# Kernel tuning notes

Hardware: AMD Instinct MI355X
Metric: run time of the kernel (lower is better)

Reference implementation:

```python
import jax, jax.numpy as jnp
import numpy as np

N_NODES = 50000
N_EDGES = 800000
IN_FEATS = 256
OUT_FEATS = 64


def setup_inputs() -> dict:
    key = jax.random.key(0)
    k1, k2, k3, k4, k5, k6 = jax.random.split(key, 6)
    h = jax.random.normal(k1, (N_NODES, IN_FEATS), dtype=jnp.float32)
    norm = jax.random.uniform(k2, (N_NODES, 1), dtype=jnp.float32)
    weight = jax.random.normal(k3, (IN_FEATS, OUT_FEATS), dtype=jnp.float32) * (1.0 / np.sqrt(OUT_FEATS))
    bias = jax.random.normal(k4, (OUT_FEATS,), dtype=jnp.float32) * (1.0 / np.sqrt(OUT_FEATS))
    src = jax.random.randint(k5, (N_EDGES,), 0, N_NODES, dtype=jnp.int32)
    dst = jax.random.randint(k6, (N_EDGES,), 0, N_NODES, dtype=jnp.int32)
    return {"h": h, "norm": norm, "weight": weight, "bias": bias, "src": src, "dst": dst}


def reference(h, norm, weight, bias, src, dst):
    # h: [N, in_feats] -> linear transform
    hw = h @ weight                      # [N, out_feats]
    hw = hw * norm                       # pre-aggregation norm scale
    # update_all(copy_u, sum): out[v] = sum_{(u,v) in E} hw[u]
    msgs = hw[src]                       # [E, out_feats] gather
    agg = jax.ops.segment_sum(msgs, dst, num_segments=N_NODES)  # [N, out_feats]
    out = agg * norm                     # post-aggregation norm scale
    out = out + bias
    return jax.nn.relu(out)
```

## Files before the change

### kernel.cpp

```cpp
#include <hip/hip_runtime.h>

#define NN 50000
#define NE 800000
#define KF 256
#define MF 64

#define NBK 782
#define SB 60
#define EPB 14336
#define EPT 14
#define CAP 1536
#define GEMMB 196
#define OVF_CAP 4096

typedef __attribute__((ext_vector_type(8))) short short8;
typedef __attribute__((ext_vector_type(4))) float f32x4;

static __device__ __forceinline__ unsigned short f2bf(float x) {
  unsigned int u = __float_as_uint(x);
  u += 0x7FFF + ((u >> 16) & 1);
  return (unsigned short)(u >> 16);
}
static __device__ __forceinline__ float bf2f(unsigned short u) {
  return __uint_as_float(((unsigned int)u) << 16);
}

__global__ __launch_bounds__(1024) void scatter_gemm(
    const int* __restrict__ src, const int* __restrict__ dst,
    int* __restrict__ gCur, int* __restrict__ gOvf,
    unsigned int* __restrict__ ovf, int* __restrict__ eidx,
    const float* __restrict__ h, const float* __restrict__ W,
    const float* __restrict__ norm, unsigned short* __restrict__ hwb) {
  const int t = threadIdx.x;

  if (blockIdx.x >= SB) {
    __shared__ unsigned short wt[16384];
    if (blockIdx.x == SB && t < 64) hwb[(size_t)NN * MF + t] = 0;
    for (int f = t; f < 2048; f += 1024) {
      const int m = f & 15;
      const int quad = (f >> 4) & 3;
      const int nt = (f >> 6) & 3;
      const int k0i = f >> 8;
      const int n = nt * 16 + m;
      const int kb = k0i * 32 + quad * 8;
      short8 p;
#pragma unroll
      for (int j = 0; j < 8; ++j) p[j] = (short)f2bf(W[(kb + j) * MF + n]);
      *(short8*)(wt + (size_t)f * 8) = p;
    }

    const int sub = t >> 8;
    const int tt = t & 255;
    const int lane = tt & 63;
    const int wv = tt >> 6;
    const int m = lane & 15;
    const int quad = lane >> 4;
    const int row0 = (blockIdx.x - SB) * 256 + sub * 64;
    const int arow = row0 + wv * 16 + m;
    const int rowc = (arow < NN) ? arow : (NN - 1);
    const float4* ap = (const float4*)(h + (size_t)rowc * KF + quad * 8);

    float4 a[16];
#pragma unroll
    for (int k = 0; k < 8; ++k) {
      a[2 * k] = ap[k * 8];
      a[2 * k + 1] = ap[k * 8 + 1];
    }
    __builtin_amdgcn_sched_barrier(0);

    short8 af[8];
#pragma unroll
    for (int k = 0; k < 8; ++k) {
      const float4 a0 = a[2 * k];
      const float4 a1 = a[2 * k + 1];
      af[k][0] = (short)f2bf(a0.x); af[k][1] = (short)f2bf(a0.y);
      af[k][2] = (short)f2bf(a0.z); af[k][3] = (short)f2bf(a0.w);
      af[k][4] = (short)f2bf(a1.x); af[k][5] = (short)f2bf(a1.y);
      af[k][6] = (short)f2bf(a1.z); af[k][7] = (short)f2bf(a1.w);
    }
    __syncthreads();

    f32x4 acc[4];
#pragma unroll
    for (int i = 0; i < 4; ++i) acc[i] = (f32x4){0.f, 0.f, 0.f, 0.f};

    const short8* wp = (const short8*)wt;
#pragma unroll
    for (int k0i = 0; k0i < 8; ++k0i) {
      const short8* wk = wp + k0i * 256 + lane;
#pragma unroll
      for (int nt = 0; nt < 4; ++nt) {
        const short8 bf = wk[nt * 64];
        acc[nt] = __builtin_amdgcn_mfma_f32_16x16x32_bf16(af[k0i], bf, acc[nt], 0, 0, 0);
      }
    }

    const int gm0 = row0 + wv * 16 + quad * 4;
    float nrm[4];
#pragma unroll
    for (int r = 0; r < 4; ++r) nrm[r] = (gm0 + r < NN) ? norm[gm0 + r] : 0.f;
#pragma unroll
    for (int nt = 0; nt < 4; ++nt) {
#pragma unroll
      for (int r = 0; r < 4; ++r) {
        const int gm = gm0 + r;
        if (gm < NN) hwb[(size_t)gm * MF + nt * 16 + m] = f2bf(acc[nt][r] * nrm[r]);
      }
    }
    return;
  }

  __shared__ int hh[NBK];
  __shared__ int bb[NBK];
  const int base = (int)blockIdx.x * EPB;
  unsigned int ev[EPT];
#pragma unroll
  for (int i = 0; i < EPT; ++i) {
    const int e = base + i * 1024 + t;
    ev[i] = (e < NE) ? (((unsigned)src[e] << 16) | (unsigned)dst[e])
                     : 0xFFFFFFFFu;
  }
  for (int i = t; i < NBK; i += 1024) hh[i] = 0;
  __syncthreads();
#pragma unroll
  for (int i = 0; i < EPT; ++i)
    if (ev[i] != 0xFFFFFFFFu) atomicAdd(&hh[(ev[i] & 0xFFFFu) >> 6], 1);
  __syncthreads();
  for (int i = t; i < NBK; i += 1024) {
    const int c = hh[i];
    bb[i] = c ? atomicAdd(&gCur[i], c) : 0;
  }
  __syncthreads();
#pragma unroll
  for (int i = 0; i < EPT; ++i) {
    const unsigned v = ev[i];
    if (v != 0xFFFFFFFFu) {
      const int d = (int)(v & 0xFFFFu);
      const int bk = d >> 6;
      const int p = atomicAdd(&bb[bk], 1);
      if (p < CAP) {
        eidx[(size_t)bk * CAP + p] = (int)((v >> 16) << 6) | (d & 63);
      } else {
        const int o = atomicAdd(gOvf, 1);
        if (o < OVF_CAP) ovf[o] = v;
      }
    }
  }
}

__global__ __launch_bounds__(1024) void sort_gather(
    const int* __restrict__ gCur, const int* __restrict__ gOvf,
    const unsigned int* __restrict__ ovf, const int* __restrict__ eidx,
    const unsigned short* __restrict__ hwb, const float* __restrict__ norm,
    const float* __restrict__ bias, float* __restrict__ out) {
  __shared__ int hcnt[64];
  __shared__ int sBeg[64];
  __shared__ int sCur[64];
  __shared__ int pEnd[64];
  __shared__ int sE[2048];
  const int t = threadIdx.x;
  const int g = blockIdx.x;
  int cnt = gCur[g];
  cnt = (cnt < CAP) ? cnt : CAP;
  cnt = __builtin_amdgcn_readfirstlane(cnt);
  const int* ep = eidx + (size_t)g * CAP;
  if (t < 64) hcnt[t] = 0;
  __syncthreads();
  int v0 = -1, v1 = -1;
  if (t < cnt) {
    v0 = ep[t];
    atomicAdd(&hcnt[v0 & 63], 1);
  }
  if (t + 1024 < cnt) {
    v1 = ep[t + 1024];
    atomicAdd(&hcnt[v1 & 63], 1);
  }
  __syncthreads();
  if (t < 64) {
    const int v = hcnt[t];
    const int pc = (v + 7) & ~7;
    int incl = pc;
#pragma unroll
    for (int off = 1; off < 64; off <<= 1) {
      const int uu = __shfl_up(incl, off, 64);
      if (t >= off) incl += uu;
    }
    const int beg = incl - pc;
    sBeg[t] = beg;
    sCur[t] = beg;
    hcnt[t] = beg + v;
    pEnd[t] = beg + pc;
  }
  __syncthreads();
  if (v0 >= 0) sE[atomicAdd(&sCur[v0 & 63], 1)] = v0 >> 6;
  if (v1 >= 0) sE[atomicAdd(&sCur[v1 & 63], 1)] = v1 >> 6;
  if (t < 64) {
    for (int j = hcnt[t]; j < pEnd[t]; ++j) sE[j] = NN;
  }
  __syncthreads();

  const int lane = t & 63;
  const int wv = t >> 6;
  const float bi = bias[lane];
  const int novf = __builtin_amdgcn_readfirstlane(*gOvf);
#pragma unroll
  for (int nl = wv; nl < 64; nl += 16) {
    const int vtx = (g << 6) + nl;
    if (vtx >= NN) continue;
    const float nv = norm[vtx];
    const int s0i = __builtin_amdgcn_readfirstlane(sBeg[nl]);
    const int e0i = __builtin_amdgcn_readfirstlane(pEnd[nl]);
    float acc = 0.f;
    int i = s0i;
    for (; i + 16 <= e0i; i += 16) {
      int ss[16];
#pragma unroll
      for (int j = 0; j < 16; ++j) ss[j] = sE[i + j];
      unsigned short xs[16];
#pragma unroll
      for (int j = 0; j < 16; ++j) xs[j] = hwb[(size_t)ss[j] * MF + lane];
      __builtin_amdgcn_sched_barrier(0);
      float p0 = 0.f, p1 = 0.f, p2 = 0.f, p3 = 0.f;
#pragma unroll
      for (int j = 0; j < 16; j += 4) {
        p0 += bf2f(xs[j]);
        p1 += bf2f(xs[j + 1]);
        p2 += bf2f(xs[j + 2]);
        p3 += bf2f(xs[j + 3]);
      }
      acc += (p0 + p1) + (p2 + p3);
    }
    if (i < e0i) {
      const int s0 = sE[i], s1 = sE[i + 1], s2 = sE[i + 2], s3 = sE[i + 3];
      const int s4 = sE[i + 4], s5 = sE[i + 5], s6 = sE[i + 6], s7 = sE[i + 7];
      const unsigned short x0 = hwb[(size_t)s0 * MF + lane];
      const unsigned short x1 = hwb[(size_t)s1 * MF + lane];
      const unsigned short x2 = hwb[(size_t)s2 * MF + lane];
      const unsigned short x3 = hwb[(size_t)s3 * MF + lane];
      const unsigned short x4 = hwb[(size_t)s4 * MF + lane];
      const unsigned short x5 = hwb[(size_t)s5 * MF + lane];
      const unsigned short x6 = hwb[(size_t)s6 * MF + lane];
      const unsigned short x7 = hwb[(size_t)s7 * MF + lane];
      acc += bf2f(x0); acc += bf2f(x1); acc += bf2f(x2); acc += bf2f(x3);
      acc += bf2f(x4); acc += bf2f(x5); acc += bf2f(x6); acc += bf2f(x7);
    }
    if (novf > 0) {
      const int nn = (novf < OVF_CAP) ? novf : OVF_CAP;
      for (int ii = 0; ii < nn; ++ii) {
        const unsigned v = ovf[ii];
        if ((int)(v & 0xFFFFu) == vtx)
          acc += bf2f(hwb[(size_t)(v >> 16) * MF + lane]);
      }
    }
    const float o = acc * nv + bi;
    out[(size_t)vtx * MF + lane] = fmaxf(o, 0.f);
  }
}

extern "C" void kernel_launch(void* const* d_in, const int* in_sizes, int n_in,
                              void* d_out, int out_size, void* d_ws, size_t ws_size,
                              hipStream_t stream) {
  const float* h = (const float*)d_in[0];
  const float* norm = (const float*)d_in[1];
  const float* W = (const float*)d_in[2];
  const float* bias = (const float*)d_in[3];
  const int* src = (const int*)d_in[4];
  const int* dst = (const int*)d_in[5];
  float* out = (float*)d_out;

  unsigned short* hwb = (unsigned short*)d_ws;
  int* gCur = (int*)(hwb + (size_t)(NN + 1) * MF);
  int* gOvf = gCur + NBK;
  unsigned int* ovf = (unsigned int*)(gOvf + 1);
  int* eidx = (int*)(ovf + OVF_CAP);
  const size_t need = (size_t)(NN + 1) * MF * 2 +
                      ((size_t)NBK + 1 + OVF_CAP + (size_t)NBK * CAP) * 4;
  if (ws_size < need) return;

  hipMemsetAsync(gCur, 0, (NBK + 1) * sizeof(int), stream);
  scatter_gemm<<<SB + GEMMB, 1024, 0, stream>>>(src, dst, gCur, gOvf, ovf,
                                                eidx, h, W, norm, hwb);
  sort_gather<<<NBK, 1024, 0, stream>>>(gCur, gOvf, ovf, eidx, hwb, norm, bias,
                                        out);
}
```

Before: 130.5 us.

## Merge scatter and GEMM roles into every block across 256 blocks

Previously 60 blocks did edge bucketing and 196 separate blocks did the bf16 MFMA GEMM. Now all 256 blocks bucket a 3125-edge slice each, and the first 196 then also run the GEMM tile, with shared memory unioned between the two phases. This spreads the serial-heavy scatter work (fewer edges per block, fewer global atomics per block) over more CUs to shorten the critical path. The cost is that GEMM blocks must finish scattering before starting their matmul, which serialises the two phases within each block.

```diff
diff --git a/kernel.cpp b/kernel.cpp
--- a/kernel.cpp
+++ b/kernel.cpp
@@ -6,9 +6,8 @@
 #define MF 64
 
 #define NBK 782
-#define SB 60
-#define EPB 14336
-#define EPT 14
+#define NB 256
+#define EPBK 3125
 #define CAP 1536
 #define GEMMB 196
 #define OVF_CAP 4096
@@ -24,6 +23,14 @@
 static __device__ __forceinline__ float bf2f(unsigned short u) {
   return __uint_as_float(((unsigned int)u) << 16);
 }
+
+union SMem1 {
+  unsigned short wt[16384];
+  struct {
+    int hh[NBK];
+    int bb[NBK];
+  } sc;
+};
 
 __global__ __launch_bounds__(1024) void scatter_gemm(
     const int* __restrict__ src, const int* __restrict__ dst,
@@ -31,119 +38,117 @@
     unsigned int* __restrict__ ovf, int* __restrict__ eidx,
     const float* __restrict__ h, const float* __restrict__ W,
     const float* __restrict__ norm, unsigned short* __restrict__ hwb) {
+  __shared__ SMem1 u;
   const int t = threadIdx.x;
 
-  if (blockIdx.x >= SB) {
-    __shared__ unsigned short wt[16384];
-    if (blockIdx.x == SB && t < 64) hwb[(size_t)NN * MF + t] = 0;
-    for (int f = t; f < 2048; f += 1024) {
-      const int m = f & 15;
-      const int quad = (f >> 4) & 3;
-      const int nt = (f >> 6) & 3;
-      const int k0i = f >> 8;
-      const int n = nt * 16 + m;
-      const int kb = k0i * 32 + quad * 8;
-      short8 p;
-#pragma unroll
-      for (int j = 0; j < 8; ++j) p[j] = (short)f2bf(W[(kb + j) * MF + n]);
-      *(short8*)(wt + (size_t)f * 8) = p;
-    }
-
-    const int sub = t >> 8;
-    const int tt = t & 255;
-    const int lane = tt & 63;
-    const int wv = tt >> 6;
-    const int m = lane & 15;
-    const int quad = lane >> 4;
-    const int row0 = (blockIdx.x - SB) * 256 + sub * 64;
-    const int arow = row0 + wv * 16 + m;
-    const int rowc = (arow < NN) ? arow : (NN - 1);
-    const float4* ap = (const float4*)(h + (size_t)rowc * KF + quad * 8);
-
-    float4 a[16];
-#pragma unroll
-    for (int k = 0; k < 8; ++k) {
-      a[2 * k] = ap[k * 8];
-      a[2 * k + 1] = ap[k * 8 + 1];
-    }
-    __builtin_amdgcn_sched_barrier(0);
-
-    short8 af[8];
-#pragma unroll
-    for (int k = 0; k < 8; ++k) {
-      const float4 a0 = a[2 * k];
-      const float4 a1 = a[2 * k + 1];
-      af[k][0] = (short)f2bf(a0.x); af[k][1] = (short)f2bf(a0.y);
-      af[k][2] = (short)f2bf(a0.z); af[k][3] = (short)f2bf(a0.w);
-      af[k][4] = (short)f2bf(a1.x); af[k][5] = (short)f2bf(a1.y);
-      af[k][6] = (short)f2bf(a1.z); af[k][7] = (short)f2bf(a1.w);
-    }
-    __syncthreads();
-
-    f32x4 acc[4];
-#pragma unroll
-    for (int i = 0; i < 4; ++i) acc[i] = (f32x4){0.f, 0.f, 0.f, 0.f};
-
-    const short8* wp = (const short8*)wt;
-#pragma unroll
-    for (int k0i = 0; k0i < 8; ++k0i) {
-      const short8* wk = wp + k0i * 256 + lane;
-#pragma unroll
-      for (int nt = 0; nt < 4; ++nt) {
-        const short8 bf = wk[nt * 64];
-        acc[nt] = __builtin_amdgcn_mfma_f32_16x16x32_bf16(af[k0i], bf, acc[nt], 0, 0, 0);
-      }
-    }
-
-    const int gm0 = row0 + wv * 16 + quad * 4;
-    float nrm[4];
-#pragma unroll
-    for (int r = 0; r < 4; ++r) nrm[r] = (gm0 + r < NN) ? norm[gm0 + r] : 0.f;
-#pragma unroll
-    for (int nt = 0; nt < 4; ++nt) {
-#pragma unroll
-      for (int r = 0; r < 4; ++r) {
-        const int gm = gm0 + r;
-        if (gm < NN) hwb[(size_t)gm * MF + nt * 16 + m] = f2bf(acc[nt][r] * nrm[r]);
-      }
-    }
-    return;
-  }
-
-  __shared__ int hh[NBK];
-  __shared__ int bb[NBK];
-  const int base = (int)blockIdx.x * EPB;
-  unsigned int ev[EPT];
-#pragma unroll
-  for (int i = 0; i < EPT; ++i) {
-    const int e = base + i * 1024 + t;
-    ev[i] = (e < NE) ? (((unsigned)src[e] << 16) | (unsigned)dst[e])
-                     : 0xFFFFFFFFu;
-  }
-  for (int i = t; i < NBK; i += 1024) hh[i] = 0;
-  __syncthreads();
-#pragma unroll
-  for (int i = 0; i < EPT; ++i)
-    if (ev[i] != 0xFFFFFFFFu) atomicAdd(&hh[(ev[i] & 0xFFFFu) >> 6], 1);
+  if (blockIdx.x == 0 && t < 64) hwb[(size_t)NN * MF + t] = 0;
+  const int base = (int)blockIdx.x * EPBK;
+  unsigned int ev[4];
+#pragma unroll
+  for (int i = 0; i < 4; ++i) {
+    const int idx = i * 1024 + t;
+    ev[i] = (idx < EPBK)
+                ? (((unsigned)src[base + idx] << 16) | (unsigned)dst[base + idx])
+                : 0xFFFFFFFFu;
+  }
+  for (int i = t; i < NBK; i += 1024) u.sc.hh[i] = 0;
+  __syncthreads();
+#pragma unroll
+  for (int i = 0; i < 4; ++i)
+    if (ev[i] != 0xFFFFFFFFu) atomicAdd(&u.sc.hh[(ev[i] & 0xFFFFu) >> 6], 1);
   __syncthreads();
   for (int i = t; i < NBK; i += 1024) {
-    const int c = hh[i];
-    bb[i] = c ? atomicAdd(&gCur[i], c) : 0;
-  }
-  __syncthreads();
-#pragma unroll
-  for (int i = 0; i < EPT; ++i) {
+    const int c = u.sc.hh[i];
+    u.sc.bb[i] = c ? atomicAdd(&gCur[i], c) : 0;
+  }
+  __syncthreads();
+#pragma unroll
+  for (int i = 0; i < 4; ++i) {
     const unsigned v = ev[i];
     if (v != 0xFFFFFFFFu) {
       const int d = (int)(v & 0xFFFFu);
       const int bk = d >> 6;
-      const int p = atomicAdd(&bb[bk], 1);
+      const int p = atomicAdd(&u.sc.bb[bk], 1);
       if (p < CAP) {
         eidx[(size_t)bk * CAP + p] = (int)((v >> 16) << 6) | (d & 63);
       } else {
         const int o = atomicAdd(gOvf, 1);
         if (o < OVF_CAP) ovf[o] = v;
       }
+    }
+  }
+  if (blockIdx.x >= GEMMB) return;
+  __syncthreads();
+
+  for (int f = t; f < 2048; f += 1024) {
+    const int m = f & 15;
+    const int quad = (f >> 4) & 3;
+    const int nt = (f >> 6) & 3;
+    const int k0i = f >> 8;
+    const int n = nt * 16 + m;
+    const int kb = k0i * 32 + quad * 8;
+    short8 p;
+#pragma unroll
+    for (int j = 0; j < 8; ++j) p[j] = (short)f2bf(W[(kb + j) * MF + n]);
+    *(short8*)(u.wt + (size_t)f * 8) = p;
+  }
+
+  const int sub = t >> 8;
+  const int tt = t & 255;
+  const int lane = tt & 63;
+  const int wv = tt >> 6;
+  const int m = lane & 15;
+  const int quad = lane >> 4;
+  const int row0 = (int)blockIdx.x * 256 + sub * 64;
+  const int arow = row0 + wv * 16 + m;
+  const int rowc = (arow < NN) ? arow : (NN - 1);
+  const float4* ap = (const float4*)(h + (size_t)rowc * KF + quad * 8);
+
+  float4 a[16];
+#pragma unroll
+  for (int k = 0; k < 8; ++k) {
+    a[2 * k] = ap[k * 8];
+    a[2 * k + 1] = ap[k * 8 + 1];
+  }
+  __builtin_amdgcn_sched_barrier(0);
+
+  short8 af[8];
+#pragma unroll
+  for (int k = 0; k < 8; ++k) {
+    const float4 a0 = a[2 * k];
+    const float4 a1 = a[2 * k + 1];
+    af[k][0] = (short)f2bf(a0.x); af[k][1] = (short)f2bf(a0.y);
+    af[k][2] = (short)f2bf(a0.z); af[k][3] = (short)f2bf(a0.w);
+    af[k][4] = (short)f2bf(a1.x); af[k][5] = (short)f2bf(a1.y);
+    af[k][6] = (short)f2bf(a1.z); af[k][7] = (short)f2bf(a1.w);
+  }
+  __syncthreads();
+
+  f32x4 acc[4];
+#pragma unroll
+  for (int i = 0; i < 4; ++i) acc[i] = (f32x4){0.f, 0.f, 0.f, 0.f};
+
+  const short8* wp = (const short8*)u.wt;
+#pragma unroll
+  for (int k0i = 0; k0i < 8; ++k0i) {
+    const short8* wk = wp + k0i * 256 + lane;
+#pragma unroll
+    for (int nt = 0; nt < 4; ++nt) {
+      const short8 bf = wk[nt * 64];
+      acc[nt] = __builtin_amdgcn_mfma_f32_16x16x32_bf16(af[k0i], bf, acc[nt], 0, 0, 0);
+    }
+  }
+
+  const int gm0 = row0 + wv * 16 + quad * 4;
+  float nrm[4];
+#pragma unroll
+  for (int r = 0; r < 4; ++r) nrm[r] = (gm0 + r < NN) ? norm[gm0 + r] : 0.f;
+#pragma unroll
+  for (int nt = 0; nt < 4; ++nt) {
+#pragma unroll
+    for (int r = 0; r < 4; ++r) {
+      const int gm = gm0 + r;
+      if (gm < NN) hwb[(size_t)gm * MF + nt * 16 + m] = f2bf(acc[nt][r] * nrm[r]);
     }
   }
 }
@@ -278,8 +283,8 @@
   if (ws_size < need) return;
 
   hipMemsetAsync(gCur, 0, (NBK + 1) * sizeof(int), stream);
-  scatter_gemm<<<SB + GEMMB, 1024, 0, stream>>>(src, dst, gCur, gOvf, ovf,
-                                                eidx, h, W, norm, hwb);
+  scatter_gemm<<<NB, 1024, 0, stream>>>(src, dst, gCur, gOvf, ovf, eidx, h, W,
+                                        norm, hwb);
   sort_gather<<<NBK, 1024, 0, stream>>>(gCur, gOvf, ovf, eidx, hwb, norm, bias,
                                         out);
 }
```

Measured after the change: 138.1 us. +5.8%, slower.

## Replace global bucket atomics with per-block fixed sub-slots and count matrix

Applied to the files above, without the earlier changes.

The scatter phase no longer reserves space with global atomics on per-bucket cursors. Each scatter block now writes into its own fixed 64-entry sub-slot per bucket and records its counts in a bucket-by-block matrix. The gather phase reads all 60 sub-slots per bucket, masked by those counts. This drops the shared histogram pass and the global atomics. In exchange each gather block scans 3840 slots instead of the actual count, and edges beyond 64 per sub-slot go to the overflow list.

```diff
diff --git a/kernel.cpp b/kernel.cpp
--- a/kernel.cpp
+++ b/kernel.cpp
@@ -9,7 +9,8 @@
 #define SB 60
 #define EPB 14336
 #define EPT 14
-#define CAP 1536
+#define SUBCAP 64
+#define SLOTS (SB * SUBCAP)
 #define GEMMB 196
 #define OVF_CAP 4096
 
@@ -25,16 +26,21 @@
   return __uint_as_float(((unsigned int)u) << 16);
 }
 
+union SMem1 {
+  unsigned short wt[16384];
+  int cur[NBK];
+};
+
 __global__ __launch_bounds__(1024) void scatter_gemm(
     const int* __restrict__ src, const int* __restrict__ dst,
-    int* __restrict__ gCur, int* __restrict__ gOvf,
+    int* __restrict__ cntM, int* __restrict__ gOvf,
     unsigned int* __restrict__ ovf, int* __restrict__ eidx,
     const float* __restrict__ h, const float* __restrict__ W,
     const float* __restrict__ norm, unsigned short* __restrict__ hwb) {
+  __shared__ SMem1 u;
   const int t = threadIdx.x;
 
   if (blockIdx.x >= SB) {
-    __shared__ unsigned short wt[16384];
     if (blockIdx.x == SB && t < 64) hwb[(size_t)NN * MF + t] = 0;
     for (int f = t; f < 2048; f += 1024) {
       const int m = f & 15;
@@ -46,7 +52,7 @@
       short8 p;
 #pragma unroll
       for (int j = 0; j < 8; ++j) p[j] = (short)f2bf(W[(kb + j) * MF + n]);
-      *(short8*)(wt + (size_t)f * 8) = p;
+      *(short8*)(u.wt + (size_t)f * 8) = p;
     }
 
     const int sub = t >> 8;
@@ -84,7 +90,7 @@
 #pragma unroll
     for (int i = 0; i < 4; ++i) acc[i] = (f32x4){0.f, 0.f, 0.f, 0.f};
 
-    const short8* wp = (const short8*)wt;
+    const short8* wp = (const short8*)u.wt;
 #pragma unroll
     for (int k0i = 0; k0i < 8; ++k0i) {
       const short8* wk = wp + k0i * 256 + lane;
@@ -110,9 +116,8 @@
     return;
   }
 
-  __shared__ int hh[NBK];
-  __shared__ int bb[NBK];
-  const int base = (int)blockIdx.x * EPB;
+  const int b = (int)blockIdx.x;
+  const int base = b * EPB;
   unsigned int ev[EPT];
 #pragma unroll
   for (int i = 0; i < EPT; ++i) {
@@ -120,16 +125,7 @@
     ev[i] = (e < NE) ? (((unsigned)src[e] << 16) | (unsigned)dst[e])
                      : 0xFFFFFFFFu;
   }
-  for (int i = t; i < NBK; i += 1024) hh[i] = 0;
-  __syncthreads();
-#pragma unroll
-  for (int i = 0; i < EPT; ++i)
-    if (ev[i] != 0xFFFFFFFFu) atomicAdd(&hh[(ev[i] & 0xFFFFu) >> 6], 1);
-  __syncthreads();
-  for (int i = t; i < NBK; i += 1024) {
-    const int c = hh[i];
-    bb[i] = c ? atomicAdd(&gCur[i], c) : 0;
-  }
+  for (int i = t; i < NBK; i += 1024) u.cur[i] = 0;
   __syncthreads();
 #pragma unroll
   for (int i = 0; i < EPT; ++i) {
@@ -137,22 +133,29 @@
     if (v != 0xFFFFFFFFu) {
       const int d = (int)(v & 0xFFFFu);
       const int bk = d >> 6;
-      const int p = atomicAdd(&bb[bk], 1);
-      if (p < CAP) {
-        eidx[(size_t)bk * CAP + p] = (int)((v >> 16) << 6) | (d & 63);
+      const int off = atomicAdd(&u.cur[bk], 1);
+      if (off < SUBCAP) {
+        eidx[(size_t)bk * SLOTS + b * SUBCAP + off] =
+            (int)((v >> 16) << 6) | (d & 63);
       } else {
         const int o = atomicAdd(gOvf, 1);
         if (o < OVF_CAP) ovf[o] = v;
       }
     }
   }
+  __syncthreads();
+  for (int k = t; k < NBK; k += 1024) {
+    const int c = u.cur[k];
+    cntM[k * 64 + b] = (c < SUBCAP) ? c : SUBCAP;
+  }
 }
 
 __global__ __launch_bounds__(1024) void sort_gather(
-    const int* __restrict__ gCur, const int* __restrict__ gOvf,
+    const int* __restrict__ cntM, const int* __restrict__ gOvf,
     const unsigned int* __restrict__ ovf, const int* __restrict__ eidx,
     const unsigned short* __restrict__ hwb, const float* __restrict__ norm,
     const float* __restrict__ bias, float* __restrict__ out) {
+  __shared__ int scnt[64];
   __shared__ int hcnt[64];
   __shared__ int sBeg[64];
   __shared__ int sCur[64];
@@ -160,20 +163,24 @@
   __shared__ int sE[2048];
   const int t = threadIdx.x;
   const int g = blockIdx.x;
-  int cnt = gCur[g];
-  cnt = (cnt < CAP) ? cnt : CAP;
-  cnt = __builtin_amdgcn_readfirstlane(cnt);
-  const int* ep = eidx + (size_t)g * CAP;
-  if (t < 64) hcnt[t] = 0;
-  __syncthreads();
-  int v0 = -1, v1 = -1;
-  if (t < cnt) {
-    v0 = ep[t];
-    atomicAdd(&hcnt[v0 & 63], 1);
-  }
-  if (t + 1024 < cnt) {
-    v1 = ep[t + 1024];
-    atomicAdd(&hcnt[v1 & 63], 1);
+  if (t < 64) {
+    scnt[t] = (t < SB) ? cntM[g * 64 + t] : 0;
+    hcnt[t] = 0;
+  }
+  __syncthreads();
+  const int* ep2 = eidx + (size_t)g * SLOTS;
+  int vv[4];
+#pragma unroll
+  for (int i = 0; i < 4; ++i) {
+    const int s = i * 1024 + t;
+    int v = -1;
+    if (s < SLOTS) {
+      const int sb = s >> 6;
+      const int off = s & 63;
+      if (off < scnt[sb]) v = ep2[s];
+    }
+    vv[i] = v;
+    if (v >= 0) atomicAdd(&hcnt[v & 63], 1);
   }
   __syncthreads();
   if (t < 64) {
@@ -192,8 +199,11 @@
     pEnd[t] = beg + pc;
   }
   __syncthreads();
-  if (v0 >= 0) sE[atomicAdd(&sCur[v0 & 63], 1)] = v0 >> 6;
-  if (v1 >= 0) sE[atomicAdd(&sCur[v1 & 63], 1)] = v1 >> 6;
+#pragma unroll
+  for (int i = 0; i < 4; ++i) {
+    const int v = vv[i];
+    if (v >= 0) sE[atomicAdd(&sCur[v & 63], 1)] = v >> 6;
+  }
   if (t < 64) {
     for (int j = hcnt[t]; j < pEnd[t]; ++j) sE[j] = NN;
   }
@@ -269,17 +279,17 @@
   float* out = (float*)d_out;
 
   unsigned short* hwb = (unsigned short*)d_ws;
-  int* gCur = (int*)(hwb + (size_t)(NN + 1) * MF);
-  int* gOvf = gCur + NBK;
+  int* cntM = (int*)(hwb + (size_t)(NN + 1) * MF);
+  int* gOvf = cntM + NBK * 64;
   unsigned int* ovf = (unsigned int*)(gOvf + 1);
   int* eidx = (int*)(ovf + OVF_CAP);
   const size_t need = (size_t)(NN + 1) * MF * 2 +
-                      ((size_t)NBK + 1 + OVF_CAP + (size_t)NBK * CAP) * 4;
+                      ((size_t)NBK * 64 + 1 + OVF_CAP + (size_t)NBK * SLOTS) * 4;
   if (ws_size < need) return;
 
-  hipMemsetAsync(gCur, 0, (NBK + 1) * sizeof(int), stream);
-  scatter_gemm<<<SB + GEMMB, 1024, 0, stream>>>(src, dst, gCur, gOvf, ovf,
+  hipMemsetAsync(gOvf, 0, sizeof(int), stream);
+  scatter_gemm<<<SB + GEMMB, 1024, 0, stream>>>(src, dst, cntM, gOvf, ovf,
                                                 eidx, h, W, norm, hwb);
-  sort_gather<<<NBK, 1024, 0, stream>>>(gCur, gOvf, ovf, eidx, hwb, norm, bias,
+  sort_gather<<<NBK, 1024, 0, stream>>>(cntM, gOvf, ovf, eidx, hwb, norm, bias,
                                         out);
 }
```

After: 133.4 us. 2.2% more time.
